# Performance work log

Hardware: AMD Instinct MI355X
Metric: run time of the kernel (lower is better)

## Reference

```python
import jax, jax.numpy as jnp
import numpy as np

CUTOFF = 5.0   # radius cutoff r
N_BASIS = 20   # radial Bessel basis size
P = 9          # polynomial cutoff degree
BOX = 40.0     # box edge length (Angstrom) for atom positions
N_ATOMS = 2048


def setup_inputs() -> dict:
    key = jax.random.key(0)
    # atoms uniformly distributed in a cubic box -> realistic sparse radius graph
    pos = jax.random.uniform(key, (N_ATOMS, 3), dtype=jnp.float32) * BOX
    return {"pos": pos}


def reference(pos):
    """EdgeEmbedding.forward (cell=None, batch=None), dense-masked jit form.

    Returns:
      dist_edge: [N, N, n_basis]  envelope(d/r) * bessel(d/r), zero outside radius/diagonal
      dir_edge:  [N, N, 3]        unit displacement vectors, zero outside radius/diagonal
      mask:      [N, N] bool      valid-edge mask (replaces dynamic edge_index)
    """
    r, p, n_basis = CUTOFF, P, N_BASIS
    n = pos.shape[0]
    disp = pos[:, None, :] - pos[None, :, :]          # [N, N, 3], disp[i,j] = pos[i]-pos[j]
    dist = jnp.sqrt(jnp.sum(disp * disp, axis=-1))    # [N, N]
    eye = jnp.eye(n, dtype=bool)
    mask = (dist < r) & (~eye)                        # RadiusGraph: i != j and |d| < r

    safe_dist = jnp.where(mask, dist, 1.0)            # avoid 0-div on diagonal / masked
    dir_edge = jnp.where(mask[..., None], disp / safe_dist[..., None], 0.0)  # ScaledNorm dir
    x = safe_dist / r                                 # ScaledNorm scaled distance

    # PolynomialCutoff: 1 - .5(p+1)(p+2)x^p + p(p+2)x^(p+1) - .5 p(p+1)x^(p+2)
    xp = x ** p
    env = 1.0 - 0.5 * (p + 1) * (p + 2) * xp + p * (p + 2) * xp * x - 0.5 * p * (p + 1) * xp * x * x

    # RadialBesselLayer: sin(k*pi*x)/x for k = 1..n_basis
    freqs = jnp.arange(1, n_basis + 1, dtype=pos.dtype) * jnp.pi  # [n_basis]
    bessel = jnp.sin(freqs * x[..., None]) / x[..., None]         # [N, N, n_basis]

    dist_edge = jnp.where(mask[..., None], env[..., None] * bessel, 0.0)
    return (dist_edge, dir_edge, mask)
```

## Files before the change

kernel.cpp:

```cpp
#include <hip/hip_runtime.h>
#include <math.h>


#define NATOMS 2048
#define NBASIS 20
#define RCUT   5.0f

__global__ __launch_bounds__(256) void edge_embed_kernel(
    const float* __restrict__ pos, float* __restrict__ out)
{
    const int t = threadIdx.x;
    const int i = blockIdx.x >> 3;
    const int j = ((blockIdx.x & 7) << 8) | t;

    const float xi = pos[3 * i + 0], yi = pos[3 * i + 1], zi = pos[3 * i + 2];
    const float xj = pos[3 * j + 0], yj = pos[3 * j + 1], zj = pos[3 * j + 2];

    const float dx = xi - xj, dy = yi - yj, dz = zi - zj;
    float d2;
    {
#pragma clang fp contract(off)
        d2 = (dx * dx + dy * dy) + dz * dz;
    }
    const float dist = sqrtf(d2);
    const bool m = (dist < RCUT) && (i != j);

    const long long pair = (long long)i * NATOMS + j;
    float* __restrict__ de  = out + pair * NBASIS;
    float* __restrict__ dir = out + (long long)NATOMS * NATOMS * NBASIS + pair * 3;
    float* __restrict__ mk  = out + (long long)NATOMS * NATOMS * (NBASIS + 3) + pair;

    float vals[NBASIS];
#pragma unroll
    for (int k = 0; k < NBASIS; ++k) vals[k] = 0.0f;
    float dirx = 0.0f, diry = 0.0f, dirz = 0.0f, mv = 0.0f;

    if (m) {
        dirx = dx / dist; diry = dy / dist; dirz = dz / dist;
        mv = 1.0f;
        const float x  = dist / RCUT;
        const float x2 = x * x, x4 = x2 * x2, x8 = x4 * x4, x9 = x8 * x;
        const float env = 1.0f - 55.0f * x9 + 99.0f * x9 * x - 45.0f * x9 * x2;
        const float theta = 3.14159265358979323846f * x;
        const float s1 = sinf(theta);
        const float c1 = cosf(theta);
        const float twoc  = 2.0f * c1;
        const float scale = env / x;
        float pm2 = 0.0f, pm1 = s1;
        vals[0] = scale * s1;
#pragma unroll
        for (int k = 1; k < NBASIS; ++k) {
            const float sk = twoc * pm1 - pm2;
            vals[k] = scale * sk;
            pm2 = pm1; pm1 = sk;
        }
    }

    float4* __restrict__ deq = (float4*)de;
#pragma unroll
    for (int q = 0; q < 5; ++q)
        deq[q] = make_float4(vals[4 * q + 0], vals[4 * q + 1], vals[4 * q + 2], vals[4 * q + 3]);
    dir[0] = dirx; dir[1] = diry; dir[2] = dirz;
    *mk = mv;
}

extern "C" void kernel_launch(void* const* d_in, const int* in_sizes, int n_in,
                              void* d_out, int out_size, void* d_ws, size_t ws_size,
                              hipStream_t stream) {
    const float* pos = (const float*)d_in[0];
    float* out = (float*)d_out;
    edge_embed_kernel<<<dim3(NATOMS * 8), dim3(256), 0, stream>>>(pos, out);
}
```

Before: 419.4 us.

## Split basis outputs across five threads per pair for coalesced float4 stores

Reassigns work so each atom pair is handled by five threads, each computing and storing one contiguous float4 chunk of the 20 Bessel values. Consecutive threads now write consecutive 16-byte segments instead of each thread writing 80 strided bytes. Direction and mask outputs are written by a subset of 64 threads per block. This adds redundant distance and sin/cos computation per thread and leaves some threads idle for the dir/mask writes.

```diff
diff --git a/kernel.cpp b/kernel.cpp
--- a/kernel.cpp
+++ b/kernel.cpp
@@ -5,17 +5,23 @@
 #define NATOMS 2048
 #define NBASIS 20
 #define RCUT   5.0f
+#define PAIRS_PER_BLOCK 64
+#define BLOCK_THREADS   320
 
-__global__ __launch_bounds__(256) void edge_embed_kernel(
+__global__ __launch_bounds__(BLOCK_THREADS) void edge_embed_kernel(
     const float* __restrict__ pos, float* __restrict__ out)
 {
     const int t = threadIdx.x;
-    const int i = blockIdx.x >> 3;
-    const int j = ((blockIdx.x & 7) << 8) | t;
+    const int blocksPerRow = NATOMS / PAIRS_PER_BLOCK;
+    const int i  = blockIdx.x / blocksPerRow;
+    const int j0 = (blockIdx.x % blocksPerRow) * PAIRS_PER_BLOCK;
+
+    const int p = t / 5;
+    const int q = t - 5 * p;
+    const int j = j0 + p;
 
     const float xi = pos[3 * i + 0], yi = pos[3 * i + 1], zi = pos[3 * i + 2];
     const float xj = pos[3 * j + 0], yj = pos[3 * j + 1], zj = pos[3 * j + 2];
-
     const float dx = xi - xj, dy = yi - yj, dz = zi - zj;
     float d2;
     {
@@ -25,43 +31,45 @@
     const float dist = sqrtf(d2);
     const bool m = (dist < RCUT) && (i != j);
 
-    const long long pair = (long long)i * NATOMS + j;
-    float* __restrict__ de  = out + pair * NBASIS;
-    float* __restrict__ dir = out + (long long)NATOMS * NATOMS * NBASIS + pair * 3;
-    float* __restrict__ mk  = out + (long long)NATOMS * NATOMS * (NBASIS + 3) + pair;
-
-    float vals[NBASIS];
-#pragma unroll
-    for (int k = 0; k < NBASIS; ++k) vals[k] = 0.0f;
-    float dirx = 0.0f, diry = 0.0f, dirz = 0.0f, mv = 0.0f;
-
+    float4 v = make_float4(0.0f, 0.0f, 0.0f, 0.0f);
     if (m) {
-        dirx = dx / dist; diry = dy / dist; dirz = dz / dist;
-        mv = 1.0f;
-        const float x  = dist / RCUT;
+        const float x  = dist * (1.0f / RCUT);
         const float x2 = x * x, x4 = x2 * x2, x8 = x4 * x4, x9 = x8 * x;
         const float env = 1.0f - 55.0f * x9 + 99.0f * x9 * x - 45.0f * x9 * x2;
+        const float scale = env / x;
         const float theta = 3.14159265358979323846f * x;
-        const float s1 = sinf(theta);
-        const float c1 = cosf(theta);
-        const float twoc  = 2.0f * c1;
-        const float scale = env / x;
-        float pm2 = 0.0f, pm1 = s1;
-        vals[0] = scale * s1;
-#pragma unroll
-        for (int k = 1; k < NBASIS; ++k) {
-            const float sk = twoc * pm1 - pm2;
-            vals[k] = scale * sk;
-            pm2 = pm1; pm1 = sk;
-        }
+        const float k0 = (float)(4 * q + 1);
+        const float s0 = sinf(k0 * theta);
+        const float s1 = sinf((k0 + 1.0f) * theta);
+        const float twoc = 2.0f * cosf(theta);
+        const float s2 = twoc * s1 - s0;
+        const float s3 = twoc * s2 - s1;
+        v = make_float4(scale * s0, scale * s1, scale * s2, scale * s3);
     }
 
-    float4* __restrict__ deq = (float4*)de;
-#pragma unroll
-    for (int q = 0; q < 5; ++q)
-        deq[q] = make_float4(vals[4 * q + 0], vals[4 * q + 1], vals[4 * q + 2], vals[4 * q + 3]);
-    dir[0] = dirx; dir[1] = diry; dir[2] = dirz;
-    *mk = mv;
+    const long long pair = (long long)i * NATOMS + j;
+    float4* __restrict__ de = (float4*)out;
+    de[pair * 5 + q] = v;
+
+    if (t < PAIRS_PER_BLOCK) {
+        const int j2 = j0 + t;
+        const float xj2 = pos[3 * j2 + 0], yj2 = pos[3 * j2 + 1], zj2 = pos[3 * j2 + 2];
+        const float ex = xi - xj2, ey = yi - yj2, ez = zi - zj2;
+        float e2;
+        {
+#pragma clang fp contract(off)
+            e2 = (ex * ex + ey * ey) + ez * ez;
+        }
+        const float ed = sqrtf(e2);
+        const bool m2 = (ed < RCUT) && (i != j2);
+        float ox = 0.0f, oy = 0.0f, oz = 0.0f, mv = 0.0f;
+        if (m2) { ox = ex / ed; oy = ey / ed; oz = ez / ed; mv = 1.0f; }
+        const long long pair2 = (long long)i * NATOMS + j2;
+        float* __restrict__ dir = out + (long long)NATOMS * NATOMS * NBASIS + pair2 * 3;
+        float* __restrict__ mk  = out + (long long)NATOMS * NATOMS * (NBASIS + 3) + pair2;
+        dir[0] = ox; dir[1] = oy; dir[2] = oz;
+        *mk = mv;
+    }
 }
 
 extern "C" void kernel_launch(void* const* d_in, const int* in_sizes, int n_in,
@@ -69,5 +77,5 @@
                               hipStream_t stream) {
     const float* pos = (const float*)d_in[0];
     float* out = (float*)d_out;
-    edge_embed_kernel<<<dim3(NATOMS * 8), dim3(256), 0, stream>>>(pos, out);
+    edge_embed_kernel<<<dim3(NATOMS * (NATOMS / PAIRS_PER_BLOCK)), dim3(BLOCK_THREADS), 0, stream>>>(pos, out);
 }
```

Result: faster. 395.6 us (-5.7%).
